# Optimization experiments

Hardware: AMD Instinct MI355X
Metric: run time of the kernel (lower is better)

## Reference

```python
import jax, jax.numpy as jnp
import numpy as np

LN_EPS = 1e-5  # torch LayerNorm default


def setup_inputs() -> dict:
    key = jax.random.key(0)
    ks = jax.random.split(key, 6)
    N, E, D = 50000, 800000, 128
    x = jax.random.normal(ks[0], (N, D), dtype=jnp.float32)
    edge_index = jax.random.randint(ks[1], (2, E), 0, N, dtype=jnp.int64)
    # Linear params (torch default-ish init scale)
    W = jax.random.normal(ks[2], (D, D), dtype=jnp.float32) / np.sqrt(D)
    b = jax.random.normal(ks[3], (D,), dtype=jnp.float32) * 0.01
    # LayerNorm params
    gamma = jnp.ones((D,), dtype=jnp.float32)
    beta = jnp.zeros((D,), dtype=jnp.float32)
    return {"x": x, "edge_index": edge_index, "W": W, "b": b,
            "gamma": gamma, "beta": beta}


def reference(x, edge_index, W, b, gamma, beta):
    N = x.shape[0]
    # add_self_loops
    loops = jnp.arange(N, dtype=edge_index.dtype)
    row = jnp.concatenate([edge_index[0], loops])  # sources (x_j)
    col = jnp.concatenate([edge_index[1], loops])  # targets (aggregate here)

    h = x @ W.T + b  # [N, D]

    # symmetric normalization: deg computed on row, includes self loops (deg>=1)
    deg = jax.ops.segment_sum(jnp.ones(row.shape, dtype=h.dtype), row,
                              num_segments=N)
    dis = deg ** -0.5
    norm = dis[row] * dis[col]  # [E+N]

    # gather-scale-scatter message passing (aggr='add')
    msg = norm[:, None] * h[row]              # [E+N, D]
    agg = jax.ops.segment_sum(msg, col, num_segments=N)  # [N, D]

    out = jax.nn.relu(agg)
    # dropout: identity (eval mode)
    mu = jnp.mean(out, axis=-1, keepdims=True)
    var = jnp.var(out, axis=-1, keepdims=True)
    out = (out - mu) * jax.lax.rsqrt(var + LN_EPS) * gamma + beta
    return out + x  # residual (in_channels == out_channels, no proj)
```

## Files before the change

kernel.cpp:

```cpp
#include <hip/hip_runtime.h>


#define D 128
#define CHSH 15
#define CHUNK (1 << CHSH)
#define NWORD 12500

typedef short bf16x8 __attribute__((ext_vector_type(8)));
typedef float f32x4 __attribute__((ext_vector_type(4)));

__device__ __forceinline__ unsigned short f2bf(float f) {
    unsigned u = __float_as_uint(f);
    return (unsigned short)((u + 0x7fffu + ((u >> 16) & 1u)) >> 16);
}
__device__ __forceinline__ float bf2f_lo(unsigned v) { return __uint_as_float(v << 16); }
__device__ __forceinline__ float bf2f_hi(unsigned v) { return __uint_as_float(v & 0xffff0000u); }

__global__ void k_cast4(const float4* __restrict__ src, ushort4* __restrict__ dst, int n4) {
    int i = blockIdx.x * 256 + threadIdx.x;
    if (i < n4) {
        float4 v = src[i];
        ushort4 o;
        o.x = f2bf(v.x); o.y = f2bf(v.y); o.z = f2bf(v.z); o.w = f2bf(v.w);
        dst[i] = o;
    }
}

__global__ void __launch_bounds__(1024)
k_gemm_hist(const float* __restrict__ x, const unsigned short* __restrict__ wb,
            const float* __restrict__ bias, unsigned short* __restrict__ hb,
            int nrows,
            const int* __restrict__ ei, int E, int n,
            unsigned char* __restrict__ degc, unsigned char* __restrict__ cntc,
            unsigned char* __restrict__ aux, int K) {
    __shared__ unsigned hist[NWORD];
    int bid = blockIdx.x;
    if (bid < 2 * K) {
        bool is_cnt = bid < K;
        int c = is_cnt ? bid : bid - K;
        const int* vs = is_cnt ? (ei + E) : ei;
        for (int i = threadIdx.x; i < NWORD; i += 1024) hist[i] = 0u;
        __syncthreads();
        int e0 = c << CHSH;
        int e1 = e0 + CHUNK; if (e1 > E) e1 = E;
        if (is_cnt) {
            for (int e = e0 + threadIdx.x; e < e1; e += 1024) {
                int v = vs[e];
                unsigned sh = (v & 3) * 8;
                unsigned old = atomicAdd(&hist[v >> 2], 1u << sh);
                aux[e] = (unsigned char)(old >> sh);
            }
        } else {
            for (int e = e0 + threadIdx.x; e < e1; e += 1024) {
                int v = vs[e];
                atomicAdd(&hist[v >> 2], 1u << ((v & 3) * 8));
            }
        }
        __syncthreads();
        unsigned* dst = (unsigned*)((is_cnt ? cntc : degc) + (size_t)c * n);
        for (int i = threadIdx.x; i < NWORD; i += 1024) dst[i] = hist[i];
    } else {
        int wid = threadIdx.x >> 6, lane = threadIdx.x & 63;
        int m0 = (bid - 2 * K) * 256 + wid * 16;
        if (m0 >= nrows) return;
        int lo16 = lane & 15, quad = lane >> 4;
        const float* arow = x + (size_t)(m0 + lo16) * D + quad * 8;
        bf16x8 a[4];
        #pragma unroll
        for (int kt = 0; kt < 4; kt++) {
            float4 p = *(const float4*)(arow + kt * 32);
            float4 q = *(const float4*)(arow + kt * 32 + 4);
            bf16x8 av;
            av[0] = (short)f2bf(p.x); av[1] = (short)f2bf(p.y);
            av[2] = (short)f2bf(p.z); av[3] = (short)f2bf(p.w);
            av[4] = (short)f2bf(q.x); av[5] = (short)f2bf(q.y);
            av[6] = (short)f2bf(q.z); av[7] = (short)f2bf(q.w);
            a[kt] = av;
        }
        #pragma unroll
        for (int nt = 0; nt < 8; nt++) {
            int n0 = nt * 16;
            const unsigned short* brow = wb + (size_t)(n0 + lo16) * D + quad * 8;
            float bj = bias[n0 + lo16];
            f32x4 acc = {bj, bj, bj, bj};
            #pragma unroll
            for (int kt = 0; kt < 4; kt++) {
                bf16x8 b = *(const bf16x8*)(brow + kt * 32);
                acc = __builtin_amdgcn_mfma_f32_16x16x32_bf16(a[kt], b, acc, 0, 0, 0);
            }
            #pragma unroll
            for (int r = 0; r < 4; r++) {
                int gr = m0 + quad * 4 + r;
                hb[(size_t)gr * D + n0 + lo16] = f2bf(acc[r]);
            }
        }
    }
}

__global__ void k_partial(const unsigned char* __restrict__ degc,
                          const unsigned char* __restrict__ cntc,
                          float* __restrict__ dis, unsigned* __restrict__ cnt,
                          unsigned* __restrict__ partial, int n, int K) {
    __shared__ unsigned s[256];
    int t = threadIdx.x;
    int i = blockIdx.x * 256 + t;
    unsigned tot = 0;
    if (i < n) {
        unsigned d = 0;
        for (int c = 0; c < K; c++) d += degc[(size_t)c * n + i];
        dis[i] = rsqrtf((float)d + 1.0f);
        for (int c = 0; c < K; c++) tot += cntc[(size_t)c * n + i];
        cnt[i] = tot;
    }
    s[t] = tot;
    __syncthreads();
    #pragma unroll
    for (int d = 128; d > 0; d >>= 1) {
        if (t < d) s[t] += s[t + d];
        __syncthreads();
    }
    if (t == 0) partial[blockIdx.x] = s[0];
}

__global__ void k_scanp(unsigned* __restrict__ partial, int nb) {
    __shared__ unsigned s[256];
    int t = threadIdx.x;
    unsigned v = (t < nb) ? partial[t] : 0u;
    s[t] = v;
    __syncthreads();
    #pragma unroll
    for (int d = 1; d < 256; d <<= 1) {
        unsigned u = (t >= d) ? s[t - d] : 0u;
        __syncthreads();
        s[t] += u;
        __syncthreads();
    }
    if (t < nb) partial[t] = s[t] - v;
}

__global__ void k_rowptrc(const unsigned* __restrict__ cnt, const unsigned char* __restrict__ cntc,
                          const unsigned* __restrict__ partial, int n, int E,
                          int* __restrict__ rowptr, int* __restrict__ rowptrc, int K) {
    __shared__ unsigned s[256];
    int t = threadIdx.x;
    int i = blockIdx.x * 256 + t;
    unsigned v = (i < n) ? cnt[i] : 0u;
    s[t] = v;
    __syncthreads();
    #pragma unroll
    for (int d = 1; d < 256; d <<= 1) {
        unsigned u = (t >= d) ? s[t - d] : 0u;
        __syncthreads();
        s[t] += u;
        __syncthreads();
    }
    if (i < n) {
        int base = (int)(partial[blockIdx.x] + s[t] - v);
        rowptr[i] = base;
        unsigned run = 0;
        for (int c = 0; c < K; c++) {
            rowptrc[(size_t)c * n + i] = base + (int)run;
            run += cntc[(size_t)c * n + i];
        }
    }
    if (blockIdx.x == 0 && t == 0) rowptr[n] = E;
}

__global__ void k_fill(const int* __restrict__ ei, int E, int n,
                       const int* __restrict__ rowptrc, const unsigned char* __restrict__ aux,
                       int* __restrict__ srcs) {
    int e = blockIdx.x * 256 + threadIdx.x;
    if (e < E) {
        int r = ei[e];
        int v = ei[E + e];
        int c = e >> CHSH;
        srcs[rowptrc[(size_t)c * n + v] + (int)aux[e]] = r;
    }
}

__global__ void k_agg(const float* __restrict__ x, const unsigned short* __restrict__ hb,
                      const float* __restrict__ dis,
                      const int* __restrict__ rowptr, const int* __restrict__ srcs,
                      const float* __restrict__ gamma, const float* __restrict__ beta,
                      float* __restrict__ out, int n) {
    int w = threadIdx.x >> 6, l = threadIdx.x & 63;
    int row = blockIdx.x * 4 + w;
    if (row >= n) return;
    const unsigned* h2 = (const unsigned*)hb;
    float dc = dis[row];
    unsigned hs = h2[(size_t)row * 64 + l];
    float accx = dc * dc * bf2f_lo(hs);
    float accy = dc * dc * bf2f_hi(hs);
    int s0 = rowptr[row], s1 = rowptr[row + 1];
    for (int base = s0; base < s1; base += 64) {
        int idx = base + l;
        int sv = (idx < s1) ? srcs[idx] : 0;
        float dv = (idx < s1) ? dis[sv] : 0.0f;
        int m = s1 - base; if (m > 64) m = 64;
        #pragma unroll 2
        for (int j = 0; j < m; j++) {
            int r = __shfl(sv, j, 64);
            float norm = dc * __shfl(dv, j, 64);
            unsigned u = h2[(size_t)r * 64 + l];
            accx += norm * bf2f_lo(u);
            accy += norm * bf2f_hi(u);
        }
    }
    float v0 = accx > 0.0f ? accx : 0.0f;
    float v1 = accy > 0.0f ? accy : 0.0f;
    float s1r = v0 + v1;
    float s2r = v0 * v0 + v1 * v1;
    #pragma unroll
    for (int m = 32; m >= 1; m >>= 1) {
        s1r += __shfl_xor(s1r, m, 64);
        s2r += __shfl_xor(s2r, m, 64);
    }
    float mean = s1r * (1.0f / 128.0f);
    float var  = s2r * (1.0f / 128.0f) - mean * mean;
    float rstd = rsqrtf(var + 1e-5f);
    float2 g  = ((const float2*)gamma)[l];
    float2 bb = ((const float2*)beta)[l];
    float2 xx = ((const float2*)x)[(size_t)row * 64 + l];
    float2 o;
    o.x = (v0 - mean) * rstd * g.x + bb.x + xx.x;
    o.y = (v1 - mean) * rstd * g.y + bb.y + xx.y;
    ((float2*)out)[(size_t)row * 64 + l] = o;
}

extern "C" void kernel_launch(void* const* d_in, const int* in_sizes, int n_in,
                              void* d_out, int out_size, void* d_ws, size_t ws_size,
                              hipStream_t stream) {
    const float* x     = (const float*)d_in[0];
    const int*   ei    = (const int*)d_in[1];
    const float* W     = (const float*)d_in[2];
    const float* bias  = (const float*)d_in[3];
    const float* gamma = (const float*)d_in[4];
    const float* beta  = (const float*)d_in[5];
    int N = in_sizes[0] / D;
    int E = in_sizes[1] / 2;
    int nb  = (N + 255) / 256;
    int nbE = (E + 255) / 256;
    int K   = (E + CHUNK - 1) >> CHSH;
    int gemm_blocks = (N + 255) / 256;

    char* ws = (char*)d_ws;
    size_t off = 0;
    unsigned short* hb  = (unsigned short*)(ws + off); off += (size_t)N * D * 2;
    unsigned short* wbf = (unsigned short*)(ws + off); off += (size_t)D * D * 2;
    unsigned char* degc = (unsigned char*)(ws + off);  off += (size_t)K * N;
    unsigned char* cntc = (unsigned char*)(ws + off);  off += (size_t)K * N;
    float*    dis       = (float*)(ws + off);          off += (size_t)N * 4;
    unsigned* cnt       = (unsigned*)(ws + off);       off += (size_t)N * 4;
    int*      rowptr    = (int*)(ws + off);            off += (size_t)(N + 1) * 4;
    int*      rowptrc   = (int*)(ws + off);            off += (size_t)K * N * 4;
    unsigned* partial   = (unsigned*)(ws + off);       off += 256 * 4;
    unsigned char* aux  = (unsigned char*)(ws + off);  off += (size_t)E;
    int*      srcs      = (int*)(ws + off);            off += (size_t)E * 4;
    float*    out       = (float*)d_out;

    k_cast4<<<(D * D / 4 + 255) / 256, 256, 0, stream>>>((const float4*)W, (ushort4*)wbf, D * D / 4);
    k_gemm_hist<<<2 * K + gemm_blocks, 1024, 0, stream>>>(x, wbf, bias, hb, N,
                                                          ei, E, N, degc, cntc, aux, K);
    k_partial<<<nb, 256, 0, stream>>>(degc, cntc, dis, cnt, partial, N, K);
    k_scanp<<<1, 256, 0, stream>>>(partial, nb);
    k_rowptrc<<<nb, 256, 0, stream>>>(cnt, cntc, partial, N, E, rowptr, rowptrc, K);
    k_fill<<<nbE, 256, 0, stream>>>(ei, E, N, rowptrc, aux, srcs);
    k_agg<<<(N + 3) / 4, 256, 0, stream>>>(x, hb, dis, rowptr, srcs, gamma, beta, out, N);
}
```

Before: 200.2 us.

## Split wavefront into four edge groups with 16-byte row gathers

The aggregation kernel now splits each 64-lane wavefront into four groups of 16 lanes. Each group processes a different neighbor edge concurrently, and each lane loads 8 bf16 values with a single 16-byte read instead of 2 values per lane. Loads are software-pipelined one edge ahead, and partial sums are combined across groups with cross-lane shuffles before ReLU and LayerNorm. The aim is more memory-level parallelism on the gather-bound loop and fewer serial shuffle/load iterations per row. The cost is 8 accumulators per lane plus extra reduction shuffles, and only a quarter of the lanes are active in the epilogue.

```diff
diff --git a/kernel.cpp b/kernel.cpp
--- a/kernel.cpp
+++ b/kernel.cpp
@@ -183,48 +183,83 @@
                       const int* __restrict__ rowptr, const int* __restrict__ srcs,
                       const float* __restrict__ gamma, const float* __restrict__ beta,
                       float* __restrict__ out, int n) {
-    int w = threadIdx.x >> 6, l = threadIdx.x & 63;
-    int row = blockIdx.x * 4 + w;
+    int wid = threadIdx.x >> 6, lane = threadIdx.x & 63;
+    int row = blockIdx.x * 4 + wid;
     if (row >= n) return;
-    const unsigned* h2 = (const unsigned*)hb;
+    int q = lane >> 4, t = lane & 15;
     float dc = dis[row];
-    unsigned hs = h2[(size_t)row * 64 + l];
-    float accx = dc * dc * bf2f_lo(hs);
-    float accy = dc * dc * bf2f_hi(hs);
-    int s0 = rowptr[row], s1 = rowptr[row + 1];
-    for (int base = s0; base < s1; base += 64) {
-        int idx = base + l;
-        int sv = (idx < s1) ? srcs[idx] : 0;
-        float dv = (idx < s1) ? dis[sv] : 0.0f;
-        int m = s1 - base; if (m > 64) m = 64;
-        #pragma unroll 2
-        for (int j = 0; j < m; j++) {
-            int r = __shfl(sv, j, 64);
-            float norm = dc * __shfl(dv, j, 64);
-            unsigned u = h2[(size_t)r * 64 + l];
-            accx += norm * bf2f_lo(u);
-            accy += norm * bf2f_hi(u);
-        }
-    }
-    float v0 = accx > 0.0f ? accx : 0.0f;
-    float v1 = accy > 0.0f ? accy : 0.0f;
-    float s1r = v0 + v1;
-    float s2r = v0 * v0 + v1 * v1;
-    #pragma unroll
-    for (int m = 32; m >= 1; m >>= 1) {
-        s1r += __shfl_xor(s1r, m, 64);
-        s2r += __shfl_xor(s2r, m, 64);
+    float acc[8];
+    #pragma unroll
+    for (int i = 0; i < 8; i++) acc[i] = 0.0f;
+    if (q == 0) {
+        uint4 u = ((const uint4*)(hb + (size_t)row * D))[t];
+        float sn = dc * dc;
+        acc[0] = sn * bf2f_lo(u.x); acc[1] = sn * bf2f_hi(u.x);
+        acc[2] = sn * bf2f_lo(u.y); acc[3] = sn * bf2f_hi(u.y);
+        acc[4] = sn * bf2f_lo(u.z); acc[5] = sn * bf2f_hi(u.z);
+        acc[6] = sn * bf2f_lo(u.w); acc[7] = sn * bf2f_hi(u.w);
+    }
+    int s0 = rowptr[row];
+    int len = rowptr[row + 1] - s0;
+    for (int base = 0; base < len; base += 64) {
+        int idx = base + lane;
+        int sv = (idx < len) ? srcs[s0 + idx] : 0;
+        float dv = (idx < len) ? dis[sv] : 0.0f;
+        int m = len - base; if (m > 64) m = 64;
+        int kmax = (m + 3) >> 2;
+        int j = q;
+        int r = __shfl(sv, j, 64);
+        float nm = dc * __shfl(dv, j, 64);
+        uint4 u = ((const uint4*)(hb + (size_t)r * D))[t];
+        for (int k = 1; k < kmax; k++) {
+            int jn = j + 4;
+            int rn = __shfl(sv, jn, 64);
+            float nmn = dc * __shfl(dv, jn, 64);
+            uint4 un = ((const uint4*)(hb + (size_t)rn * D))[t];
+            acc[0] += nm * bf2f_lo(u.x); acc[1] += nm * bf2f_hi(u.x);
+            acc[2] += nm * bf2f_lo(u.y); acc[3] += nm * bf2f_hi(u.y);
+            acc[4] += nm * bf2f_lo(u.z); acc[5] += nm * bf2f_hi(u.z);
+            acc[6] += nm * bf2f_lo(u.w); acc[7] += nm * bf2f_hi(u.w);
+            u = un; nm = nmn; j = jn;
+        }
+        acc[0] += nm * bf2f_lo(u.x); acc[1] += nm * bf2f_hi(u.x);
+        acc[2] += nm * bf2f_lo(u.y); acc[3] += nm * bf2f_hi(u.y);
+        acc[4] += nm * bf2f_lo(u.z); acc[5] += nm * bf2f_hi(u.z);
+        acc[6] += nm * bf2f_lo(u.w); acc[7] += nm * bf2f_hi(u.w);
+    }
+    #pragma unroll
+    for (int i = 0; i < 8; i++) {
+        acc[i] += __shfl_xor(acc[i], 16, 64);
+        acc[i] += __shfl_xor(acc[i], 32, 64);
+        acc[i] = acc[i] > 0.0f ? acc[i] : 0.0f;
+    }
+    float s1r = 0.0f, s2r = 0.0f;
+    #pragma unroll
+    for (int i = 0; i < 8; i++) { s1r += acc[i]; s2r += acc[i] * acc[i]; }
+    #pragma unroll
+    for (int mm = 8; mm >= 1; mm >>= 1) {
+        s1r += __shfl_xor(s1r, mm, 64);
+        s2r += __shfl_xor(s2r, mm, 64);
     }
     float mean = s1r * (1.0f / 128.0f);
     float var  = s2r * (1.0f / 128.0f) - mean * mean;
     float rstd = rsqrtf(var + 1e-5f);
-    float2 g  = ((const float2*)gamma)[l];
-    float2 bb = ((const float2*)beta)[l];
-    float2 xx = ((const float2*)x)[(size_t)row * 64 + l];
-    float2 o;
-    o.x = (v0 - mean) * rstd * g.x + bb.x + xx.x;
-    o.y = (v1 - mean) * rstd * g.y + bb.y + xx.y;
-    ((float2*)out)[(size_t)row * 64 + l] = o;
+    if (q == 0) {
+        const float4* gr = (const float4*)gamma;
+        const float4* br = (const float4*)beta;
+        const float4* xr = (const float4*)(x + (size_t)row * D);
+        float4* orow = (float4*)(out + (size_t)row * D);
+        #pragma unroll
+        for (int hf = 0; hf < 2; hf++) {
+            float4 g = gr[2 * t + hf], b = br[2 * t + hf], xx = xr[2 * t + hf];
+            float4 o;
+            o.x = (acc[4 * hf + 0] - mean) * rstd * g.x + b.x + xx.x;
+            o.y = (acc[4 * hf + 1] - mean) * rstd * g.y + b.y + xx.y;
+            o.z = (acc[4 * hf + 2] - mean) * rstd * g.z + b.z + xx.z;
+            o.w = (acc[4 * hf + 3] - mean) * rstd * g.w + b.w + xx.w;
+            orow[2 * t + hf] = o;
+        }
+    }
 }
 
 extern "C" void kernel_launch(void* const* d_in, const int* in_sizes, int n_in,
```

After: 183.2 us. 1.09x faster.
